# Kernel optimization log

Measured on AMD Instinct MI355X. Metric: run time of the kernel, lower is better.

## Reference

```python
import jax, jax.numpy as jnp
import numpy as np

N_HEADS = 8
TOP_K = 100


def setup_inputs() -> dict:
    key = jax.random.key(0)
    ks = jax.random.split(key, 12)
    B, S, H, U = 16, 2048, 1024, 512
    s = 0.02
    return {
        "query": jax.random.normal(ks[0], (B, H), jnp.float32),
        "values": jax.random.normal(ks[1], (B, S, H), jnp.float32),
        # stacked per-head Bahdanau params (8 heads)
        "W1": jax.random.normal(ks[2], (N_HEADS, H, U), jnp.float32) * s,
        "b1": jnp.zeros((N_HEADS, U), jnp.float32),
        "W2": jax.random.normal(ks[3], (N_HEADS, H, U), jnp.float32) * s,
        "b2": jnp.zeros((N_HEADS, U), jnp.float32),
        "Vw": jax.random.normal(ks[4], (N_HEADS, U), jnp.float32) * s,
        "Vb": jnp.zeros((N_HEADS,), jnp.float32),
        # head-mixing linear W: nbr_heads -> 1
        "Ww": jax.random.normal(ks[5], (N_HEADS,), jnp.float32) * s,
        "Wb": jnp.zeros((), jnp.float32),
    }


def reference(query, values, W1, b1, W2, b2, Vw, Vb, Ww, Wb):
    # per-head additive attention scores, vectorized over the 8 heads
    # values: [B,S,H], query: [B,H]
    hid = jnp.tanh(
        jnp.einsum('bsh,nhu->nbsu', values, W1) + b1[:, None, None, :]
        + jnp.einsum('bh,nhu->nbu', query, W2)[:, :, None, :] + b2[:, None, None, :]
    )  # [N,B,S,U]
    scores = jnp.einsum('nbsu,nu->bsn', hid, Vw) + Vb  # [B,S,N] == concat of 8 head scores
    score = jnp.einsum('bsn,n->bs', scores, Ww) + Wb   # [B,S]

    # topk over sequence dim, then zero all non-topk positions:
    # torch: score = -(score.scatter(1, top_pos, 0) - score)
    _, top_pos = jax.lax.top_k(score, TOP_K)           # [B,K]
    bidx = jnp.arange(score.shape[0])[:, None]
    sc0 = score.at[bidx, top_pos].set(0.0)
    masked = (score - sc0)[..., None]                  # [B,S,1]: topk vals kept, 0 else

    # custom sigmoid 'softmax' normalized over the BATCH dim (dim 0), as in source
    w = jax.nn.sigmoid(masked)
    w = w / w.sum(0)                                   # [B,S,1]
    context = (w * values).sum(1)                      # [B,H]
    return context, w, masked
```

## Files before the change

kernel.cpp:

```cpp
#include <hip/hip_runtime.h>
#include <hip/hip_bf16.h>

#define B_ 16
#define S_ 2048
#define H_ 1024
#define U_ 512
#define NH 8
#define TOPK 100

#define M_ (B_*S_)
#define NC (NH*U_)

typedef int i32x4 __attribute__((ext_vector_type(4)));

__device__ __forceinline__ float fast_tanh(float x) {
    float e = __expf(2.f * x);
    return (e - 1.f) / (e + 1.f);
}

__device__ __forceinline__ void gl16i(const signed char* g, signed char* l) {
    __builtin_amdgcn_global_load_lds(
        (const __attribute__((address_space(1))) void*)g,
        (__attribute__((address_space(3))) void*)l, 16, 0, 0);
}

__global__ void cvtA(const float* __restrict__ v,
                     signed char* __restrict__ h8,
                     float* __restrict__ sa) {
    int row = blockIdx.x * 4 + (threadIdx.x >> 6);
    int l = threadIdx.x & 63;
    const float4* r4 = (const float4*)(v + (size_t)row * 1024);
    float4 x[4];
    float mx = 0.f;
    #pragma unroll
    for (int c = 0; c < 4; ++c) {
        x[c] = r4[l * 4 + c];
        mx = fmaxf(mx, fmaxf(fmaxf(fabsf(x[c].x), fabsf(x[c].y)),
                             fmaxf(fabsf(x[c].z), fabsf(x[c].w))));
    }
    #pragma unroll
    for (int d = 1; d < 64; d <<= 1) mx = fmaxf(mx, __shfl_xor(mx, d));
    float inv = 127.f / mx;
    int wh[4];
    #pragma unroll
    for (int c = 0; c < 4; ++c) {
        float xs[4] = {x[c].x, x[c].y, x[c].z, x[c].w};
        unsigned ph = 0;
        #pragma unroll
        for (int j = 0; j < 4; ++j) {
            float hf = rintf(xs[j] * inv);
            ph |= ((unsigned)((int)hf) & 0xffu) << (8 * j);
        }
        wh[c] = (int)ph;
    }
    *(int4*)(h8 + (size_t)row * 1024 + l * 16) = make_int4(wh[0], wh[1], wh[2], wh[3]);
    if (l == 0) sa[row] = mx / 127.f;
}

__global__ void colmax_kernel(const float* __restrict__ W1, float* __restrict__ cm) {
    int n = blockIdx.x, h0 = blockIdx.y * 64, u = threadIdx.x;
    const float* p = W1 + ((size_t)n * H_ + h0) * U_ + u;
    float mx = 0.f;
    #pragma unroll 8
    for (int h = 0; h < 64; ++h) mx = fmaxf(mx, fabsf(p[(size_t)h * U_]));
    atomicMax((unsigned*)(cm + n * U_ + u), __float_as_uint(mx));
}

__global__ void cvtB8(const float* __restrict__ W1,
                      const float* __restrict__ cm,
                      signed char* __restrict__ bh) {
    __shared__ float t[64][65];
    int n = blockIdx.x, h0 = blockIdx.y * 64, u0 = blockIdx.z * 64;
    int tid = threadIdx.x;
    int ul = tid & 63;
    #pragma unroll
    for (int i = 0; i < 16; ++i) {
        int hl = i * 4 + (tid >> 6);
        t[hl][ul] = W1[((size_t)n * H_ + h0 + hl) * U_ + u0 + ul];
    }
    __syncthreads();
    #pragma unroll
    for (int i = 0; i < 16; ++i) {
        int ulw = i * 4 + (tid >> 6);
        int hlw = tid & 63;
        float q = t[hlw][ulw] * (127.f / cm[n * 512 + u0 + ulw]);
        size_t o = ((size_t)(n * 512 + u0 + ulw)) * 1024 + h0 + hlw;
        bh[o] = (signed char)(int)rintf(q);
    }
}

__global__ void qbp_kernel(const float* __restrict__ query,
                           const float* __restrict__ W2,
                           float* __restrict__ qbp) {
    int n = blockIdx.x, hc = blockIdx.y;
    int u = threadIdx.x;
    int h0 = hc * 64;
    __shared__ float q[16][64];
    #pragma unroll
    for (int k = 0; k < 2; ++k) {
        int idx = threadIdx.x + k * 512;
        q[idx >> 6][idx & 63] = query[(idx >> 6) * H_ + h0 + (idx & 63)];
    }
    __syncthreads();
    float acc[16];
    #pragma unroll
    for (int b = 0; b < 16; ++b) acc[b] = 0.f;
    const float* w2 = W2 + ((size_t)n * H_ + h0) * U_ + u;
    #pragma unroll 4
    for (int hh = 0; hh < 64; ++hh) {
        float wv = w2[(size_t)hh * U_];
        #pragma unroll
        for (int b = 0; b < 16; ++b) acc[b] = fmaf(q[b][hh], wv, acc[b]);
    }
    float* dst = qbp + ((size_t)hc * NH + n) * 16 * U_ + u;
    #pragma unroll
    for (int b = 0; b < 16; ++b) dst[(size_t)b * U_] = acc[b];
}

__global__ void qb_reduce(const float* __restrict__ qbp,
                          const float* __restrict__ b1,
                          const float* __restrict__ b2,
                          float* __restrict__ qb) {
    int i = blockIdx.x * 256 + threadIdx.x;
    int n = i >> 13;
    int u = i & 511;
    float s = b1[n * U_ + u] + b2[n * U_ + u];
    #pragma unroll
    for (int hc = 0; hc < 16; ++hc) s += qbp[(size_t)hc * 65536 + i];
    qb[i] = s;
}

#define NT 16
#define SWZ(d) ((d) ^ ((((d) >> 7) & 3) << 4))
#define K0B(tt) ((tt) * 64)
#define STAGE_A(tt, j) gl16i(Ah8 + (size_t)(rowBase + (j)*128 + rT) * 1024 + K0B(tt) + cTb, \
                             lds + ((tt)&3)*32768 + (j)*8192 + tid*16)
#define STAGE_B(tt, j) gl16i(Bh8 + (size_t)(colBase + (j)*128 + rT) * 1024 + K0B(tt) + cTb, \
                             lds + ((tt)&3)*32768 + 16384 + (j)*8192 + tid*16)

__global__ __launch_bounds__(512, 1) void gemm8i(
        const signed char* __restrict__ Ah8,
        const signed char* __restrict__ Bh8,
        const float* __restrict__ sa, const float* __restrict__ cm,
        const float* __restrict__ qb, const float* __restrict__ Vw,
        const float* __restrict__ Ww, float* __restrict__ partial) {
    __shared__ signed char lds[131072];
    const int tid = threadIdx.x;
    const int lane = tid & 63;
    const int wid = tid >> 6;
    const int wm = wid >> 2, wn = wid & 3;
    int bid = blockIdx.x;
    int swz = (bid & 7) * 256 + (bid >> 3);
    int mIdx = swz & 127, nIdx = swz >> 7;
    int rowBase = mIdx * 256, colBase = nIdx * 256;

    int d0 = tid * 16;
    int d0s = SWZ(d0);
    int rT  = d0s >> 6;
    int cTb = d0s & 63;

    const int l15 = lane & 15, l4 = lane >> 4;
    int offA[8], offB[4];
    #pragma unroll
    for (int m = 0; m < 8; ++m)
        offA[m] = SWZ((wm * 128 + m * 16 + l15) * 64 + l4 * 16);
    #pragma unroll
    for (int n = 0; n < 4; ++n)
        offB[n] = 16384 + SWZ((wn * 64 + n * 16 + l15) * 64 + l4 * 16);

    i32x4 acc[8][4];
    #pragma unroll
    for (int m = 0; m < 8; ++m)
        #pragma unroll
        for (int n = 0; n < 4; ++n) acc[m][n] = (i32x4){0, 0, 0, 0};

    #pragma unroll
    for (int tt = 0; tt < 3; ++tt) {
        STAGE_A(tt, 0); STAGE_A(tt, 1);
        STAGE_B(tt, 0); STAGE_B(tt, 1);
    }
    asm volatile("s_waitcnt vmcnt(8)" ::: "memory");
    __builtin_amdgcn_s_barrier();

    #pragma unroll 1
    for (int t = 0; t < NT; ++t) {
        __builtin_amdgcn_sched_barrier(0);
        if (t <= NT - 4) {
            STAGE_A(t + 3, 0); STAGE_A(t + 3, 1);
            STAGE_B(t + 3, 0); STAGE_B(t + 3, 1);
        }
        const signed char* slot = lds + (t & 3) * 32768;
        i32x4 bf[4], af[8];
        #pragma unroll
        for (int n = 0; n < 4; ++n) bf[n] = *(const i32x4*)(slot + offB[n]);
        #pragma unroll
        for (int m = 0; m < 8; ++m) af[m] = *(const i32x4*)(slot + offA[m]);
        #pragma unroll
        for (int m = 0; m < 8; ++m)
            #pragma unroll
            for (int n = 0; n < 4; ++n)
                acc[m][n] = __builtin_amdgcn_mfma_i32_16x16x64_i8(af[m], bf[n], acc[m][n], 0, 0, 0);
        asm volatile("s_waitcnt lgkmcnt(0)" ::: "memory");
        if (t <= NT - 4)      asm volatile("s_waitcnt vmcnt(8)" ::: "memory");
        else if (t == NT - 3) asm volatile("s_waitcnt vmcnt(4)" ::: "memory");
        else if (t == NT - 2) asm volatile("s_waitcnt vmcnt(0)" ::: "memory");
        __builtin_amdgcn_s_barrier();
    }

    __syncthreads();
    int hd = colBase >> 9;
    int b = rowBase >> 11;
    float wwn = Ww[hd];
    float qv[4], vw[4], sbv[4];
    #pragma unroll
    for (int n = 0; n < 4; ++n) {
        int col = colBase + wn * 64 + n * 16 + l15;
        int u = col & 511;
        qv[n] = qb[((size_t)hd * B_ + b) * U_ + u];
        vw[n] = Vw[hd * U_ + u] * wwn;
        sbv[n] = cm[col] * (1.f / 127.f);
    }
    float* red = (float*)lds;
    #pragma unroll
    for (int m = 0; m < 8; ++m) {
        float sav[4];
        #pragma unroll
        for (int r = 0; r < 4; ++r)
            sav[r] = sa[rowBase + wm * 128 + m * 16 + l4 * 4 + r];
        #pragma unroll
        for (int r = 0; r < 4; ++r) {
            float p = 0.f;
            #pragma unroll
            for (int n = 0; n < 4; ++n)
                p += vw[n] * fast_tanh((float)acc[m][n][r] * sav[r] * sbv[n] + qv[n]);
            p += __shfl_xor(p, 1);
            p += __shfl_xor(p, 2);
            p += __shfl_xor(p, 4);
            p += __shfl_xor(p, 8);
            if (l15 == 0)
                red[wn * 256 + wm * 128 + m * 16 + l4 * 4 + r] = p;
        }
    }
    __syncthreads();
    if (tid < 256) {
        float s = red[tid] + red[256 + tid] + red[512 + tid] + red[768 + tid];
        partial[(size_t)nIdx * M_ + rowBase + tid] = s;
    }
}

__global__ __launch_bounds__(256, 2) void gemm_score(
        const float* __restrict__ values,
        const float* __restrict__ W1,
        const float* __restrict__ qb,
        const float* __restrict__ Vw,
        const float* __restrict__ Ww,
        float* __restrict__ partial) {
    __shared__ float As[16][128 + 4];
    __shared__ float Bs[16][128 + 4];
    int tid = threadIdx.x;
    int tx = tid & 15, ty = tid >> 4;
    int rowBase = blockIdx.x * 128;
    int colBase = blockIdx.y * 128;
    int n = colBase >> 9;
    int u0 = colBase & 511;
    int b = rowBase >> 11;
    float acc[8][8];
    #pragma unroll
    for (int i = 0; i < 8; ++i)
        #pragma unroll
        for (int j = 0; j < 8; ++j) acc[i][j] = 0.f;
    const float* Ag = values + (size_t)rowBase * H_;
    const float* Bg = W1 + (size_t)n * H_ * U_ + u0;
    for (int k0 = 0; k0 < H_; k0 += 16) {
        #pragma unroll
        for (int r = 0; r < 2; ++r) {
            int idx = tid + r * 256;
            int arow = idx >> 2, aqc = idx & 3;
            float4 v = *(const float4*)(Ag + (size_t)arow * H_ + k0 + aqc * 4);
            As[aqc * 4 + 0][arow] = v.x;
            As[aqc * 4 + 1][arow] = v.y;
            As[aqc * 4 + 2][arow] = v.z;
            As[aqc * 4 + 3][arow] = v.w;
        }
        #pragma unroll
        for (int r = 0; r < 2; ++r) {
            int idx = tid + r * 256;
            int bk = idx >> 5, bqc = idx & 31;
            float4 v = *(const float4*)(Bg + (size_t)(k0 + bk) * U_ + bqc * 4);
            *(float4*)&Bs[bk][bqc * 4] = v;
        }
        __syncthreads();
        #pragma unroll
        for (int k = 0; k < 16; ++k) {
            float4 a0 = *(const float4*)&As[k][ty * 8];
            float4 a1 = *(const float4*)&As[k][ty * 8 + 4];
            float4 b0 = *(const float4*)&Bs[k][tx * 8];
            float4 b1v = *(const float4*)&Bs[k][tx * 8 + 4];
            float av[8] = {a0.x, a0.y, a0.z, a0.w, a1.x, a1.y, a1.z, a1.w};
            float bv[8] = {b0.x, b0.y, b0.z, b0.w, b1v.x, b1v.y, b1v.z, b1v.w};
            #pragma unroll
            for (int i = 0; i < 8; ++i)
                #pragma unroll
                for (int j = 0; j < 8; ++j)
                    acc[i][j] = fmaf(av[i], bv[j], acc[i][j]);
        }
        __syncthreads();
    }
    float qbv[8], vwv[8];
    #pragma unroll
    for (int j = 0; j < 8; ++j) {
        int u = u0 + tx * 8 + j;
        qbv[j] = qb[(n * B_ + b) * U_ + u];
        vwv[j] = Vw[n * U_ + u];
    }
    float wwn = Ww[n];
    #pragma unroll
    for (int i = 0; i < 8; ++i) {
        float p = 0.f;
        #pragma unroll
        for (int j = 0; j < 8; ++j)
            p += vwv[j] * fast_tanh(acc[i][j] + qbv[j]);
        p += __shfl_xor(p, 1);
        p += __shfl_xor(p, 2);
        p += __shfl_xor(p, 4);
        p += __shfl_xor(p, 8);
        if (tx == 0)
            partial[(size_t)blockIdx.y * M_ + rowBase + ty * 8 + i] = wwn * p;
    }
}

__global__ __launch_bounds__(1024) void topk_kernel(
        const float* __restrict__ partial, int nparts,
        const float* __restrict__ Vb,
        const float* __restrict__ Ww,
        const float* __restrict__ Wb,
        float* __restrict__ out_masked,
        float* __restrict__ w_un) {
    __shared__ float sc[S_];
    __shared__ float srt[S_];
    __shared__ int cnt_gt;
    int b = blockIdx.x;
    int tid = threadIdx.x;
    float cst = Wb[0];
    #pragma unroll
    for (int n2 = 0; n2 < NH; ++n2) cst += Ww[n2] * Vb[n2];
    for (int s = tid; s < S_; s += 1024) {
        float v = cst;
        for (int ct = 0; ct < nparts; ++ct)
            v += partial[(size_t)ct * M_ + b * S_ + s];
        sc[s] = v; srt[s] = v;
    }
    if (tid == 0) cnt_gt = 0;
    __syncthreads();
    for (int k = 2; k <= S_; k <<= 1) {
        for (int j = k >> 1; j >= 1; j >>= 1) {
            int i = ((tid & ~(j - 1)) << 1) | (tid & (j - 1));
            int p = i | j;
            float a = srt[i], c2 = srt[p];
            if (((i & k) == 0) ? (a > c2) : (a < c2)) { srt[i] = c2; srt[p] = a; }
            __syncthreads();
        }
    }
    float T = srt[S_ - TOPK];
    int c = 0;
    for (int s = tid; s < S_; s += 1024) c += (sc[s] > T);
    atomicAdd(&cnt_gt, c);
    __syncthreads();
    int need_eq = TOPK - cnt_gt;
    for (int s = tid; s < S_; s += 1024) {
        float v = sc[s];
        bool sel = (v > T);
        if (v == T) {
            int rank = 0;
            for (int t2 = 0; t2 < s; ++t2) rank += (sc[t2] == T);
            sel = (rank < need_eq);
        }
        float m = sel ? v : 0.f;
        out_masked[b * S_ + s] = m;
        w_un[b * S_ + s] = 1.f / (1.f + __expf(-m));
    }
}

__global__ void norm_w(const float* __restrict__ w_un, float* __restrict__ out_w) {
    int s = blockIdx.x * blockDim.x + threadIdx.x;
    float d = 0.f;
    #pragma unroll
    for (int b = 0; b < B_; ++b) d += w_un[b * S_ + s];
    float inv = 1.f / d;
    #pragma unroll
    for (int b = 0; b < B_; ++b) out_w[b * S_ + s] = w_un[b * S_ + s] * inv;
}

__global__ void ctx_partial_h8(const signed char* __restrict__ h8,
                               const float* __restrict__ sa,
                               const float* __restrict__ w,
                               float* __restrict__ pctx) {
    int bb = blockIdx.x;
    int h = blockIdx.y * 256 + threadIdx.x;
    int s0 = blockIdx.z * 256;
    __shared__ float ws[256];
    {
        int s = threadIdx.x;
        ws[s] = w[bb * S_ + s0 + s] * sa[bb * S_ + s0 + s];
    }
    __syncthreads();
    const signed char* hp = h8 + (size_t)(bb * S_ + s0) * H_ + h;
    float acc = 0.f;
    #pragma unroll 4
    for (int s = 0; s < 256; ++s)
        acc += ws[s] * (float)hp[(size_t)s * H_];
    pctx[((size_t)blockIdx.z * B_ + bb) * H_ + h] = acc;
}

__global__ void ctx_partial_f32(const float* __restrict__ values,
                                const float* __restrict__ w,
                                float* __restrict__ pctx) {
    int bb = blockIdx.x;
    int h = blockIdx.y * 256 + threadIdx.x;
    int s0 = blockIdx.z * 256;
    __shared__ float wrow[256];
    wrow[threadIdx.x] = w[bb * S_ + s0 + threadIdx.x];
    __syncthreads();
    const float* vp = values + (size_t)(bb * S_ + s0) * H_ + h;
    float acc = 0.f;
    #pragma unroll 4
    for (int s = 0; s < 256; ++s) acc += wrow[s] * vp[(size_t)s * H_];
    pctx[((size_t)blockIdx.z * B_ + bb) * H_ + h] = acc;
}

__global__ void ctx_reduce(const float* __restrict__ pctx,
                           float* __restrict__ out_ctx) {
    int i = blockIdx.x * blockDim.x + threadIdx.x;
    float s = 0.f;
    #pragma unroll
    for (int z = 0; z < 8; ++z) s += pctx[(size_t)z * B_ * H_ + i];
    out_ctx[i] = s;
}

extern "C" void kernel_launch(void* const* d_in, const int* in_sizes, int n_in,
                              void* d_out, int out_size, void* d_ws, size_t ws_size,
                              hipStream_t stream) {
    const float* query = (const float*)d_in[0];
    const float* values = (const float*)d_in[1];
    const float* W1 = (const float*)d_in[2];
    const float* b1 = (const float*)d_in[3];
    const float* W2 = (const float*)d_in[4];
    const float* b2 = (const float*)d_in[5];
    const float* Vw = (const float*)d_in[6];
    const float* Vb = (const float*)d_in[7];
    const float* Ww = (const float*)d_in[8];
    const float* Wb = (const float*)d_in[9];

    float* ws = (float*)d_ws;
    float* qb      = ws;
    float* qbp     = qb + 65536;
    float* partial = qbp + 1048576;
    float* w_un    = partial + 1048576;
    float* pctx    = w_un + 32768;
    float* sa      = pctx + 131072;
    float* colmax  = sa + 32768;
    signed char* Ah8 = (signed char*)(colmax + 4096);
    signed char* Bh8 = Ah8 + (size_t)M_ * H_;
    size_t needed = (size_t)((char*)(Bh8 + (size_t)NC * H_) - (char*)d_ws);

    float* out_ctx    = (float*)d_out;
    float* out_w      = out_ctx + 16384;
    float* out_masked = out_w + 32768;

    qbp_kernel<<<dim3(NH, 16), 512, 0, stream>>>(query, W2, qbp);
    qb_reduce<<<dim3(256), 256, 0, stream>>>(qbp, b1, b2, qb);
    if (ws_size >= needed) {
        cvtA<<<dim3(8192), 256, 0, stream>>>(values, Ah8, sa);
        hipMemsetAsync(colmax, 0, NC * sizeof(float), stream);
        colmax_kernel<<<dim3(NH, 16), 512, 0, stream>>>(W1, colmax);
        cvtB8<<<dim3(NH, 16, 8), 256, 0, stream>>>(W1, colmax, Bh8);
        gemm8i<<<dim3(2048), 512, 0, stream>>>(Ah8, Bh8, sa, colmax,
                                               qb, Vw, Ww, partial);
        topk_kernel<<<16, 1024, 0, stream>>>(partial, 16, Vb, Ww, Wb, out_masked, w_un);
        norm_w<<<8, 256, 0, stream>>>(w_un, out_w);
        ctx_partial_h8<<<dim3(16, 4, 8), 256, 0, stream>>>(Ah8, sa, out_w, pctx);
    } else {
        gemm_score<<<dim3(256, 32), 256, 0, stream>>>(values, W1, qb, Vw, Ww, partial);
        topk_kernel<<<16, 1024, 0, stream>>>(partial, 32, Vb, Ww, Wb, out_masked, w_un);
        norm_w<<<8, 256, 0, stream>>>(w_un, out_w);
        ctx_partial_f32<<<dim3(16, 4, 8), 256, 0, stream>>>(values, out_w, pctx);
    }
    ctx_reduce<<<64, 256, 0, stream>>>(pctx, out_ctx);
}
```

Before: 400.5 us.

## Process two K-tiles per barrier with prefetch distance two in int8 GEMM

The int8 MFMA main loop used a 3-deep prefetch with one barrier per K-tile. It now handles two tiles per iteration: each tile issues its global-to-LDS loads two tiles ahead, and the loop waits with vmcnt(0) and one barrier after every pair. The sched_barrier and the post-loop __syncthreads are removed. This halves the number of barriers and waitcnt points, at the cost of a shallower prefetch distance and a full vmcnt drain each pair, which may expose more global load latency.

Measured after the change: 398.1 us. About the same (-0.6%).

```diff
diff --git a/kernel.cpp b/kernel.cpp
--- a/kernel.cpp
+++ b/kernel.cpp
@@ -137,6 +137,24 @@
                              lds + ((tt)&3)*32768 + (j)*8192 + tid*16)
 #define STAGE_B(tt, j) gl16i(Bh8 + (size_t)(colBase + (j)*128 + rT) * 1024 + K0B(tt) + cTb, \
                              lds + ((tt)&3)*32768 + 16384 + (j)*8192 + tid*16)
+
+#define ITER2(T) do {                                                         \
+    if ((T) <= NT - 3) {                                                      \
+        STAGE_A((T) + 2, 0); STAGE_A((T) + 2, 1);                             \
+        STAGE_B((T) + 2, 0); STAGE_B((T) + 2, 1);                             \
+    }                                                                         \
+    const signed char* slot_ = lds + ((T) & 3) * 32768;                       \
+    i32x4 bf_[4], af_[8];                                                     \
+    _Pragma("unroll")                                                         \
+    for (int n = 0; n < 4; ++n) bf_[n] = *(const i32x4*)(slot_ + offB[n]);    \
+    _Pragma("unroll")                                                         \
+    for (int m = 0; m < 8; ++m) af_[m] = *(const i32x4*)(slot_ + offA[m]);    \
+    _Pragma("unroll")                                                         \
+    for (int m = 0; m < 8; ++m)                                               \
+      _Pragma("unroll")                                                       \
+      for (int n = 0; n < 4; ++n)                                             \
+        acc[m][n] = __builtin_amdgcn_mfma_i32_16x16x64_i8(af_[m], bf_[n], acc[m][n], 0, 0, 0); \
+  } while (0)
 
 __global__ __launch_bounds__(512, 1) void gemm8i(
         const signed char* __restrict__ Ah8,
@@ -174,40 +192,20 @@
         #pragma unroll
         for (int n = 0; n < 4; ++n) acc[m][n] = (i32x4){0, 0, 0, 0};
 
-    #pragma unroll
-    for (int tt = 0; tt < 3; ++tt) {
-        STAGE_A(tt, 0); STAGE_A(tt, 1);
-        STAGE_B(tt, 0); STAGE_B(tt, 1);
-    }
-    asm volatile("s_waitcnt vmcnt(8)" ::: "memory");
+    STAGE_A(0, 0); STAGE_A(0, 1); STAGE_B(0, 0); STAGE_B(0, 1);
+    STAGE_A(1, 0); STAGE_A(1, 1); STAGE_B(1, 0); STAGE_B(1, 1);
+    asm volatile("s_waitcnt vmcnt(0)" ::: "memory");
     __builtin_amdgcn_s_barrier();
 
     #pragma unroll 1
-    for (int t = 0; t < NT; ++t) {
-        __builtin_amdgcn_sched_barrier(0);
-        if (t <= NT - 4) {
-            STAGE_A(t + 3, 0); STAGE_A(t + 3, 1);
-            STAGE_B(t + 3, 0); STAGE_B(t + 3, 1);
-        }
-        const signed char* slot = lds + (t & 3) * 32768;
-        i32x4 bf[4], af[8];
-        #pragma unroll
-        for (int n = 0; n < 4; ++n) bf[n] = *(const i32x4*)(slot + offB[n]);
-        #pragma unroll
-        for (int m = 0; m < 8; ++m) af[m] = *(const i32x4*)(slot + offA[m]);
-        #pragma unroll
-        for (int m = 0; m < 8; ++m)
-            #pragma unroll
-            for (int n = 0; n < 4; ++n)
-                acc[m][n] = __builtin_amdgcn_mfma_i32_16x16x64_i8(af[m], bf[n], acc[m][n], 0, 0, 0);
+    for (int t = 0; t < NT; t += 2) {
+        ITER2(t);
+        ITER2(t + 1);
         asm volatile("s_waitcnt lgkmcnt(0)" ::: "memory");
-        if (t <= NT - 4)      asm volatile("s_waitcnt vmcnt(8)" ::: "memory");
-        else if (t == NT - 3) asm volatile("s_waitcnt vmcnt(4)" ::: "memory");
-        else if (t == NT - 2) asm volatile("s_waitcnt vmcnt(0)" ::: "memory");
+        asm volatile("s_waitcnt vmcnt(0)" ::: "memory");
         __builtin_amdgcn_s_barrier();
     }
 
-    __syncthreads();
     int hd = colBase >> 9;
     int b = rowBase >> 11;
     float wwn = Ww[hd];
```
